# Kernel optimization log

Hardware: AMD Instinct MI355X
Metric: run time of the kernel (lower is better)

The kernel has to match this reference:

```python
import jax, jax.numpy as jnp
import numpy as np

E = 8        # num_local_experts
H = 2048     # hidden_size
I = 4096     # intermediate_size
TOP_K = 1    # num_experts_per_tok
B, S = 2, 1024


def setup_inputs() -> dict:
    key = jax.random.key(0)
    ks = jax.random.split(key, 8)
    sc = 0.02
    return {
        "hidden_states": jax.random.normal(ks[0], (B, S, H), dtype=jnp.float32),
        "router_w": jax.random.normal(ks[1], (E, H), dtype=jnp.float32) * sc,      # torch Linear weight [out,in]
        "gate_up_proj": jax.random.normal(ks[2], (E, H, 2 * I), dtype=jnp.float32) * sc,
        "down_proj": jax.random.normal(ks[3], (E, I, H), dtype=jnp.float32) * sc,
        "shared_gate": jax.random.normal(ks[4], (H, I), dtype=jnp.float32) * sc,
        "shared_up": jax.random.normal(ks[5], (H, I), dtype=jnp.float32) * sc,
        "shared_down": jax.random.normal(ks[6], (I, H), dtype=jnp.float32) * sc,
    }


def reference(hidden_states, router_w, gate_up_proj, down_proj, shared_gate, shared_up, shared_down):
    x = hidden_states.reshape(-1, H)                      # [T, H]
    T = x.shape[0]

    # Router: top-k logits kept, rest -> -inf, then sigmoid (Llama4 sigmoid routing)
    logits = jnp.einsum('th,eh->te', x, router_w)          # [T, E]
    topv, topi = jax.lax.top_k(logits, TOP_K)
    scores = jnp.full_like(logits, -jnp.inf)
    scores = scores.at[jnp.arange(T)[:, None], topi].set(topv)
    router_scores = jax.nn.sigmoid(scores.astype(jnp.float32)).astype(x.dtype).T  # [E, T]

    # Dense dispatch: every token goes to every expert, scaled by its (mostly-zero) score
    routed_in = x[None, :, :] * router_scores[:, :, None]  # [E, T, H]

    # Per-expert gated MLP as one grouped einsum
    gu = jnp.einsum('eth,ehf->etf', routed_in, gate_up_proj)   # [E, T, 2I]
    gate, up = gu[..., :I], gu[..., I:]
    routed_out = jnp.einsum('eti,eih->eth', jax.nn.silu(gate) * up, down_proj)  # [E, T, H]

    # Shared expert on raw tokens
    shared = (jax.nn.silu(x @ shared_gate) * (x @ shared_up)) @ shared_down     # [T, H]

    # scatter_add over full index range == sum over expert axis
    out = shared + routed_out.sum(axis=0)
    return out, router_scores
```

## Files before the change

### kernel.cpp

```cpp
#include <hip/hip_runtime.h>
#include <hip/hip_bf16.h>

#define NE 8
#define TT 2048
#define HD 2048
#define ID 4096

typedef __attribute__((ext_vector_type(8))) short bf16x8;
typedef __attribute__((ext_vector_type(4))) float f32x4;
typedef __attribute__((ext_vector_type(4))) unsigned int u32x4;
typedef __attribute__((ext_vector_type(2))) unsigned int u32x2;
typedef __attribute__((ext_vector_type(4))) unsigned short u16x4;

__device__ __forceinline__ unsigned short f2bf(float f) {
  unsigned int u = __builtin_bit_cast(unsigned int, f);
  u += 0x7FFFu + ((u >> 16) & 1u);
  return (unsigned short)(u >> 16);
}

__global__ void init_kernel(int* counts) {
  if (threadIdx.x < NE) counts[threadIdx.x] = 0;
}

__global__ __launch_bounds__(256) void router_kernel(
    const float* __restrict__ x, const float* __restrict__ rw,
    float* __restrict__ rs_out, unsigned short* __restrict__ xb,
    unsigned short* __restrict__ xsb, int* __restrict__ counts,
    int* __restrict__ tlist) {
  const int t = blockIdx.x;
  const int tid = threadIdx.x;
  const float* xr = x + (size_t)t * HD;
  float acc[NE];
#pragma unroll
  for (int e = 0; e < NE; ++e) acc[e] = 0.f;
  for (int h = tid; h < HD; h += 256) {
    float xv = xr[h];
#pragma unroll
    for (int e = 0; e < NE; ++e) acc[e] += xv * rw[e * HD + h];
  }
#pragma unroll
  for (int e = 0; e < NE; ++e) {
#pragma unroll
    for (int off = 32; off > 0; off >>= 1) acc[e] += __shfl_down(acc[e], off);
  }
  __shared__ float part[4][NE];
  __shared__ int sE;
  __shared__ float sS;
  const int wave = tid >> 6, lane = tid & 63;
  if (lane == 0) {
#pragma unroll
    for (int e = 0; e < NE; ++e) part[wave][e] = acc[e];
  }
  __syncthreads();
  if (tid == 0) {
    float best = -3.4e38f;
    int be = 0;
#pragma unroll
    for (int e = 0; e < NE; ++e) {
      float v = part[0][e] + part[1][e] + part[2][e] + part[3][e];
      if (v > best) { best = v; be = e; }
    }
    float s = 1.f / (1.f + expf(-best));
    sE = be;
    sS = s;
    int pos = atomicAdd(&counts[be], 1);
    tlist[be * TT + pos] = t;
  }
  __syncthreads();
  if (tid < NE) rs_out[tid * TT + t] = (tid == sE) ? sS : 0.f;
  const float s = sS;
  for (int h = tid; h < HD; h += 256) {
    float f = xr[h];
    xb[(size_t)t * HD + h] = f2bf(f);
    xsb[(size_t)t * HD + h] = f2bf(f * s);
  }
}

__global__ __launch_bounds__(256) void gateup_kernel(
    const unsigned short* __restrict__ xb, const unsigned short* __restrict__ xsb,
    const float* __restrict__ gup, const float* __restrict__ shg,
    const float* __restrict__ shu, const int* __restrict__ counts,
    const int* __restrict__ tlist, unsigned short* __restrict__ hsh,
    unsigned short* __restrict__ hrt) {
  const int bz = blockIdx.z;
  const bool sh = (bz == NE);
  const int cnt = sh ? TT : counts[bz];
  const int row0 = blockIdx.y * 128;
  if (row0 >= cnt) return;
  const int n0 = blockIdx.x * 64;
  const unsigned short* Aptr = sh ? xb : xsb;
  const float* B1;
  const float* B2;
  size_t ldb;
  if (sh) {
    B1 = shg + n0; B2 = shu + n0; ldb = ID;
  } else {
    const float* base = gup + (size_t)bz * HD * 2 * ID;
    B1 = base + n0; B2 = base + ID + n0; ldb = 2 * ID;
  }
  unsigned short* hout = sh ? hsh : hrt;

  __shared__ int toks[128];
  __shared__ __align__(16) unsigned short As[128][40];
  __shared__ __align__(16) unsigned short Bg[64][36];
  __shared__ __align__(16) unsigned short Bu[64][36];

  const int tid = threadIdx.x;
  if (tid < 128) {
    int r = row0 + tid;
    toks[tid] = (r < cnt) ? (sh ? r : tlist[bz * TT + r]) : -1;
  }
  __syncthreads();

  const int lane = tid & 63;
  const int wave = tid >> 6;
  const int wm = (wave >> 1) * 64, wn = (wave & 1) * 32;
  const int rA0 = tid >> 2, cA = (tid & 3) * 8, rA1 = rA0 + 64;
  const int tok0 = toks[rA0], tok1 = toks[rA1];
  const int nB = tid & 63;
  const int fm = lane & 15, q = lane >> 4;

  const f32x4 zf = {0.f, 0.f, 0.f, 0.f};
  f32x4 accg[4][2], accu[4][2];
#pragma unroll
  for (int a = 0; a < 4; ++a)
#pragma unroll
    for (int b = 0; b < 2; ++b) { accg[a][b] = zf; accu[a][b] = zf; }

  for (int k0 = 0; k0 < HD; k0 += 32) {
    u32x4 v0 = {0, 0, 0, 0}, v1 = {0, 0, 0, 0};
    if (tok0 >= 0) v0 = *(const u32x4*)(const void*)(Aptr + (size_t)tok0 * HD + k0 + cA);
    if (tok1 >= 0) v1 = *(const u32x4*)(const void*)(Aptr + (size_t)tok1 * HD + k0 + cA);
    *(u32x4*)(void*)&As[rA0][cA] = v0;
    *(u32x4*)(void*)&As[rA1][cA] = v1;
#pragma unroll
    for (int i = 0; i < 2; ++i) {
      const int kq = (tid >> 6) + 4 * i;
      const float* p1 = B1 + (size_t)(k0 + kq * 4) * ldb + nB;
      u16x4 w1;
      w1[0] = f2bf(p1[0]); w1[1] = f2bf(p1[ldb]);
      w1[2] = f2bf(p1[2 * ldb]); w1[3] = f2bf(p1[3 * ldb]);
      *(u16x4*)(void*)&Bg[nB][kq * 4] = w1;
      const float* p2 = B2 + (size_t)(k0 + kq * 4) * ldb + nB;
      u16x4 w2;
      w2[0] = f2bf(p2[0]); w2[1] = f2bf(p2[ldb]);
      w2[2] = f2bf(p2[2 * ldb]); w2[3] = f2bf(p2[3 * ldb]);
      *(u16x4*)(void*)&Bu[nB][kq * 4] = w2;
    }
    __syncthreads();
    bf16x8 af[4];
#pragma unroll
    for (int mt = 0; mt < 4; ++mt)
      af[mt] = __builtin_bit_cast(bf16x8,
               *(const u32x4*)(const void*)&As[wm + mt * 16 + fm][q * 8]);
    bf16x8 bgf[2], buf2[2];
#pragma unroll
    for (int nt = 0; nt < 2; ++nt) {
      const unsigned short* bp = &Bg[wn + nt * 16 + fm][q * 8];
      u32x2 lo = *(const u32x2*)(const void*)bp;
      u32x2 hi = *(const u32x2*)(const void*)(bp + 4);
      u32x4 v; v[0] = lo[0]; v[1] = lo[1]; v[2] = hi[0]; v[3] = hi[1];
      bgf[nt] = __builtin_bit_cast(bf16x8, v);
      const unsigned short* bp2 = &Bu[wn + nt * 16 + fm][q * 8];
      lo = *(const u32x2*)(const void*)bp2;
      hi = *(const u32x2*)(const void*)(bp2 + 4);
      v[0] = lo[0]; v[1] = lo[1]; v[2] = hi[0]; v[3] = hi[1];
      buf2[nt] = __builtin_bit_cast(bf16x8, v);
    }
#pragma unroll
    for (int mt = 0; mt < 4; ++mt)
#pragma unroll
      for (int nt = 0; nt < 2; ++nt) {
        accg[mt][nt] = __builtin_amdgcn_mfma_f32_16x16x32_bf16(af[mt], bgf[nt], accg[mt][nt], 0, 0, 0);
        accu[mt][nt] = __builtin_amdgcn_mfma_f32_16x16x32_bf16(af[mt], buf2[nt], accu[mt][nt], 0, 0, 0);
      }
    __syncthreads();
  }
#pragma unroll
  for (int mt = 0; mt < 4; ++mt)
#pragma unroll
    for (int nt = 0; nt < 2; ++nt)
#pragma unroll
      for (int r = 0; r < 4; ++r) {
        int ml = wm + mt * 16 + q * 4 + r;
        if (row0 + ml < cnt) {
          int tok = toks[ml];
          int n = n0 + wn + nt * 16 + fm;
          float g = accg[mt][nt][r], u = accu[mt][nt][r];
          float hv = g / (1.f + __expf(-g)) * u;
          hout[(size_t)tok * ID + n] = f2bf(hv);
        }
      }
}

__global__ __launch_bounds__(256) void down_kernel(
    const unsigned short* __restrict__ Ah, const float* __restrict__ Bbase,
    const int* __restrict__ counts, const int* __restrict__ tlist,
    float* __restrict__ out, const int routed) {
  const int e = blockIdx.z;
  const int cnt = routed ? counts[e] : TT;
  const int row0 = blockIdx.y * 128;
  if (row0 >= cnt) return;
  const int n0 = blockIdx.x * 64;
  const float* B = routed ? (Bbase + (size_t)e * ID * HD + n0) : (Bbase + n0);

  __shared__ int toks[128];
  __shared__ __align__(16) unsigned short As[128][40];
  __shared__ __align__(16) unsigned short Bs[64][36];

  const int tid = threadIdx.x;
  if (tid < 128) {
    int r = row0 + tid;
    toks[tid] = (r < cnt) ? (routed ? tlist[e * TT + r] : r) : -1;
  }
  __syncthreads();

  const int lane = tid & 63, wave = tid >> 6;
  const int wm = (wave >> 1) * 64, wn = (wave & 1) * 32;
  const int rA0 = tid >> 2, cA = (tid & 3) * 8, rA1 = rA0 + 64;
  const int tok0 = toks[rA0], tok1 = toks[rA1];
  const int nB = tid & 63;
  const int fm = lane & 15, q = lane >> 4;

  const f32x4 zf = {0.f, 0.f, 0.f, 0.f};
  f32x4 acc[4][2];
#pragma unroll
  for (int a = 0; a < 4; ++a)
#pragma unroll
    for (int b = 0; b < 2; ++b) acc[a][b] = zf;

  for (int k0 = 0; k0 < ID; k0 += 32) {
    u32x4 v0 = {0, 0, 0, 0}, v1 = {0, 0, 0, 0};
    if (tok0 >= 0) v0 = *(const u32x4*)(const void*)(Ah + (size_t)tok0 * ID + k0 + cA);
    if (tok1 >= 0) v1 = *(const u32x4*)(const void*)(Ah + (size_t)tok1 * ID + k0 + cA);
    *(u32x4*)(void*)&As[rA0][cA] = v0;
    *(u32x4*)(void*)&As[rA1][cA] = v1;
#pragma unroll
    for (int i = 0; i < 2; ++i) {
      const int kq = (tid >> 6) + 4 * i;
      const float* p = B + (size_t)(k0 + kq * 4) * HD + nB;
      u16x4 w;
      w[0] = f2bf(p[0]); w[1] = f2bf(p[HD]);
      w[2] = f2bf(p[2 * HD]); w[3] = f2bf(p[3 * HD]);
      *(u16x4*)(void*)&Bs[nB][kq * 4] = w;
    }
    __syncthreads();
    bf16x8 af[4];
#pragma unroll
    for (int mt = 0; mt < 4; ++mt)
      af[mt] = __builtin_bit_cast(bf16x8,
               *(const u32x4*)(const void*)&As[wm + mt * 16 + fm][q * 8]);
    bf16x8 bfr[2];
#pragma unroll
    for (int nt = 0; nt < 2; ++nt) {
      const unsigned short* bp = &Bs[wn + nt * 16 + fm][q * 8];
      u32x2 lo = *(const u32x2*)(const void*)bp;
      u32x2 hi = *(const u32x2*)(const void*)(bp + 4);
      u32x4 v; v[0] = lo[0]; v[1] = lo[1]; v[2] = hi[0]; v[3] = hi[1];
      bfr[nt] = __builtin_bit_cast(bf16x8, v);
    }
#pragma unroll
    for (int mt = 0; mt < 4; ++mt)
#pragma unroll
      for (int nt = 0; nt < 2; ++nt)
        acc[mt][nt] = __builtin_amdgcn_mfma_f32_16x16x32_bf16(af[mt], bfr[nt], acc[mt][nt], 0, 0, 0);
    __syncthreads();
  }
#pragma unroll
  for (int mt = 0; mt < 4; ++mt)
#pragma unroll
    for (int nt = 0; nt < 2; ++nt)
#pragma unroll
      for (int r = 0; r < 4; ++r) {
        int ml = wm + mt * 16 + q * 4 + r;
        if (row0 + ml < cnt) {
          int tok = toks[ml];
          int n = n0 + wn + nt * 16 + fm;
          float v = acc[mt][nt][r];
          float* o = out + (size_t)tok * HD + n;
          if (routed) *o += v; else *o = v;
        }
      }
}

extern "C" void kernel_launch(void* const* d_in, const int* in_sizes, int n_in,
                              void* d_out, int out_size, void* d_ws, size_t ws_size,
                              hipStream_t stream) {
  const float* x   = (const float*)d_in[0];
  const float* rw  = (const float*)d_in[1];
  const float* gup = (const float*)d_in[2];
  const float* dwn = (const float*)d_in[3];
  const float* shg = (const float*)d_in[4];
  const float* shu = (const float*)d_in[5];
  const float* shd = (const float*)d_in[6];
  float* out = (float*)d_out;

  char* ws = (char*)d_ws;
  int* counts = (int*)ws;
  int* tlist = (int*)(ws + 1024);
  unsigned short* xb  = (unsigned short*)(ws + (1 << 17));
  unsigned short* xsb = (unsigned short*)(ws + (1 << 17) + 8388608);
  unsigned short* hsh = (unsigned short*)(ws + (1 << 17) + 16777216);
  unsigned short* hrt = (unsigned short*)(ws + (1 << 17) + 33554432);

  hipLaunchKernelGGL(init_kernel, dim3(1), dim3(64), 0, stream, counts);
  hipLaunchKernelGGL(router_kernel, dim3(TT), dim3(256), 0, stream,
                     x, rw, out + (size_t)TT * HD, xb, xsb, counts, tlist);
  hipLaunchKernelGGL(gateup_kernel, dim3(ID / 64, TT / 128, NE + 1), dim3(256), 0, stream,
                     xb, xsb, gup, shg, shu, counts, tlist, hsh, hrt);
  hipLaunchKernelGGL(down_kernel, dim3(HD / 64, TT / 128, 1), dim3(256), 0, stream,
                     hsh, shd, counts, tlist, out, 0);
  hipLaunchKernelGGL(down_kernel, dim3(HD / 64, TT / 128, NE), dim3(256), 0, stream,
                     hrt, dwn, counts, tlist, out, 1);
}
```

Baseline: 1.447 ms.

## Double-buffer GEMM LDS tiles and pre-convert shared-expert weights to transposed bf16

Both GEMM kernels now keep two LDS buffers and prefetch global data two K-steps ahead into registers, so each K-step needs one barrier instead of two, and wave priority is raised around the MFMA block. A new conversion kernel transposes the shared-expert weights into bf16 once per call. The shared-expert B tiles are then read with 16-byte loads instead of strided fp32 loads converted in-loop. LDS row padding changes so B fragments can be read with a single 16-byte load. This costs an extra conversion pass over the three shared weight matrices and more workspace, and it is only enabled when the workspace is large enough.

After: 1.351 ms. 1.07x faster.

```diff
diff --git a/kernel.cpp b/kernel.cpp
--- a/kernel.cpp
+++ b/kernel.cpp
@@ -9,8 +9,8 @@
 typedef __attribute__((ext_vector_type(8))) short bf16x8;
 typedef __attribute__((ext_vector_type(4))) float f32x4;
 typedef __attribute__((ext_vector_type(4))) unsigned int u32x4;
-typedef __attribute__((ext_vector_type(2))) unsigned int u32x2;
 typedef __attribute__((ext_vector_type(4))) unsigned short u16x4;
+typedef __attribute__((ext_vector_type(8))) unsigned short u16x8;
 
 __device__ __forceinline__ unsigned short f2bf(float f) {
   unsigned int u = __builtin_bit_cast(unsigned int, f);
@@ -76,12 +76,49 @@
   }
 }
 
+__global__ __launch_bounds__(256) void tconv_kernel(
+    const float* __restrict__ shg, const float* __restrict__ shu,
+    const float* __restrict__ shd, unsigned short* __restrict__ shgT,
+    unsigned short* __restrict__ shuT, unsigned short* __restrict__ shdT) {
+  const int z = blockIdx.z;
+  const float* src;
+  unsigned short* dst;
+  int K, N;
+  if (z == 0)      { src = shg; dst = shgT; K = HD; N = ID; }
+  else if (z == 1) { src = shu; dst = shuT; K = HD; N = ID; }
+  else             { src = shd; dst = shdT; K = ID; N = HD; }
+  const int kb = blockIdx.y * 64, nb = blockIdx.x * 64;
+  if (kb >= K || nb >= N) return;
+  __shared__ unsigned short tile[64][68];
+  const int tid = threadIdx.x;
+  const int rr = tid >> 4, cc = (tid & 15) * 4;
+#pragma unroll
+  for (int it = 0; it < 4; ++it) {
+    int r = rr + it * 16;
+    f32x4 v = *(const f32x4*)(const void*)(src + (size_t)(kb + r) * N + nb + cc);
+    tile[r][cc + 0] = f2bf(v[0]);
+    tile[r][cc + 1] = f2bf(v[1]);
+    tile[r][cc + 2] = f2bf(v[2]);
+    tile[r][cc + 3] = f2bf(v[3]);
+  }
+  __syncthreads();
+  const int nr = tid >> 2, kc = (tid & 3) * 16;
+#pragma unroll
+  for (int h = 0; h < 2; ++h) {
+    u16x8 w;
+#pragma unroll
+    for (int j = 0; j < 8; ++j) w[j] = tile[kc + h * 8 + j][nr];
+    *(u16x8*)(void*)(dst + (size_t)(nb + nr) * K + kb + kc + h * 8) = w;
+  }
+}
+
 __global__ __launch_bounds__(256) void gateup_kernel(
     const unsigned short* __restrict__ xb, const unsigned short* __restrict__ xsb,
     const float* __restrict__ gup, const float* __restrict__ shg,
-    const float* __restrict__ shu, const int* __restrict__ counts,
+    const float* __restrict__ shu, const unsigned short* __restrict__ shgT,
+    const unsigned short* __restrict__ shuT, const int* __restrict__ counts,
     const int* __restrict__ tlist, unsigned short* __restrict__ hsh,
-    unsigned short* __restrict__ hrt) {
+    unsigned short* __restrict__ hrt, const int shbf) {
   const int bz = blockIdx.z;
   const bool sh = (bz == NE);
   const int cnt = sh ? TT : counts[bz];
@@ -89,11 +126,13 @@
   if (row0 >= cnt) return;
   const int n0 = blockIdx.x * 64;
   const unsigned short* Aptr = sh ? xb : xsb;
-  const float* B1;
-  const float* B2;
+  const bool bfb = sh && (shbf != 0);
+  const float *B1, *B2;
   size_t ldb;
+  const unsigned short *T1 = nullptr, *T2 = nullptr;
   if (sh) {
     B1 = shg + n0; B2 = shu + n0; ldb = ID;
+    T1 = shgT + (size_t)n0 * HD; T2 = shuT + (size_t)n0 * HD;
   } else {
     const float* base = gup + (size_t)bz * HD * 2 * ID;
     B1 = base + n0; B2 = base + ID + n0; ldb = 2 * ID;
@@ -101,9 +140,9 @@
   unsigned short* hout = sh ? hsh : hrt;
 
   __shared__ int toks[128];
-  __shared__ __align__(16) unsigned short As[128][40];
-  __shared__ __align__(16) unsigned short Bg[64][36];
-  __shared__ __align__(16) unsigned short Bu[64][36];
+  __shared__ __align__(16) unsigned short As[2][128][40];
+  __shared__ __align__(16) unsigned short Bg[2][64][40];
+  __shared__ __align__(16) unsigned short Bu[2][64][40];
 
   const int tid = threadIdx.x;
   if (tid < 128) {
@@ -112,61 +151,91 @@
   }
   __syncthreads();
 
-  const int lane = tid & 63;
-  const int wave = tid >> 6;
+  const int lane = tid & 63, wave = tid >> 6;
   const int wm = (wave >> 1) * 64, wn = (wave & 1) * 32;
   const int rA0 = tid >> 2, cA = (tid & 3) * 8, rA1 = rA0 + 64;
   const int tok0 = toks[rA0], tok1 = toks[rA1];
+  const unsigned short* ap0 = Aptr + ((tok0 >= 0) ? (size_t)tok0 * HD : 0) + cA;
+  const unsigned short* ap1 = Aptr + ((tok1 >= 0) ? (size_t)tok1 * HD : 0) + cA;
   const int nB = tid & 63;
+  const int kq0 = tid >> 6;
   const int fm = lane & 15, q = lane >> 4;
+  const int nrT = tid >> 2, kcT = (tid & 3) * 8;
 
   const f32x4 zf = {0.f, 0.f, 0.f, 0.f};
+  const u32x4 z4 = {0u, 0u, 0u, 0u};
   f32x4 accg[4][2], accu[4][2];
 #pragma unroll
   for (int a = 0; a < 4; ++a)
 #pragma unroll
     for (int b = 0; b < 2; ++b) { accg[a][b] = zf; accu[a][b] = zf; }
 
-  for (int k0 = 0; k0 < HD; k0 += 32) {
-    u32x4 v0 = {0, 0, 0, 0}, v1 = {0, 0, 0, 0};
-    if (tok0 >= 0) v0 = *(const u32x4*)(const void*)(Aptr + (size_t)tok0 * HD + k0 + cA);
-    if (tok1 >= 0) v1 = *(const u32x4*)(const void*)(Aptr + (size_t)tok1 * HD + k0 + cA);
-    *(u32x4*)(void*)&As[rA0][cA] = v0;
-    *(u32x4*)(void*)&As[rA1][cA] = v1;
-#pragma unroll
-    for (int i = 0; i < 2; ++i) {
-      const int kq = (tid >> 6) + 4 * i;
-      const float* p1 = B1 + (size_t)(k0 + kq * 4) * ldb + nB;
-      u16x4 w1;
-      w1[0] = f2bf(p1[0]); w1[1] = f2bf(p1[ldb]);
-      w1[2] = f2bf(p1[2 * ldb]); w1[3] = f2bf(p1[3 * ldb]);
-      *(u16x4*)(void*)&Bg[nB][kq * 4] = w1;
-      const float* p2 = B2 + (size_t)(k0 + kq * 4) * ldb + nB;
-      u16x4 w2;
-      w2[0] = f2bf(p2[0]); w2[1] = f2bf(p2[ldb]);
-      w2[2] = f2bf(p2[2 * ldb]); w2[3] = f2bf(p2[3 * ldb]);
-      *(u16x4*)(void*)&Bu[nB][kq * 4] = w2;
-    }
-    __syncthreads();
-    bf16x8 af[4];
+  u32x4 ra0, ra1, tb1, tb2;
+  f32x4 rg0, rg1, ru0, ru1;
+
+#define GU_LOAD(K0)                                                            \
+  do {                                                                         \
+    ra0 = (tok0 >= 0) ? *(const u32x4*)(const void*)(ap0 + (K0)) : z4;         \
+    ra1 = (tok1 >= 0) ? *(const u32x4*)(const void*)(ap1 + (K0)) : z4;         \
+    if (bfb) {                                                                 \
+      tb1 = *(const u32x4*)(const void*)(T1 + (size_t)nrT * HD + (K0) + kcT);  \
+      tb2 = *(const u32x4*)(const void*)(T2 + (size_t)nrT * HD + (K0) + kcT);  \
+    } else {                                                                   \
+      const float* p1 = B1 + (size_t)((K0) + kq0 * 4) * ldb + nB;              \
+      const float* p1b = p1 + 16 * ldb;                                        \
+      rg0[0] = p1[0]; rg0[1] = p1[ldb]; rg0[2] = p1[2 * ldb]; rg0[3] = p1[3 * ldb]; \
+      rg1[0] = p1b[0]; rg1[1] = p1b[ldb]; rg1[2] = p1b[2 * ldb]; rg1[3] = p1b[3 * ldb]; \
+      const float* p2 = B2 + (size_t)((K0) + kq0 * 4) * ldb + nB;              \
+      const float* p2b = p2 + 16 * ldb;                                        \
+      ru0[0] = p2[0]; ru0[1] = p2[ldb]; ru0[2] = p2[2 * ldb]; ru0[3] = p2[3 * ldb]; \
+      ru1[0] = p2b[0]; ru1[1] = p2b[ldb]; ru1[2] = p2b[2 * ldb]; ru1[3] = p2b[3 * ldb]; \
+    }                                                                          \
+  } while (0)
+
+#define GU_WRITE(BUF)                                                          \
+  do {                                                                         \
+    *(u32x4*)(void*)&As[BUF][rA0][cA] = ra0;                                   \
+    *(u32x4*)(void*)&As[BUF][rA1][cA] = ra1;                                   \
+    if (bfb) {                                                                 \
+      *(u32x4*)(void*)&Bg[BUF][nrT][kcT] = tb1;                                \
+      *(u32x4*)(void*)&Bu[BUF][nrT][kcT] = tb2;                                \
+    } else {                                                                   \
+      u16x4 w;                                                                 \
+      w[0] = f2bf(rg0[0]); w[1] = f2bf(rg0[1]); w[2] = f2bf(rg0[2]); w[3] = f2bf(rg0[3]); \
+      *(u16x4*)(void*)&Bg[BUF][nB][kq0 * 4] = w;                               \
+      w[0] = f2bf(rg1[0]); w[1] = f2bf(rg1[1]); w[2] = f2bf(rg1[2]); w[3] = f2bf(rg1[3]); \
+      *(u16x4*)(void*)&Bg[BUF][nB][kq0 * 4 + 16] = w;                          \
+      w[0] = f2bf(ru0[0]); w[1] = f2bf(ru0[1]); w[2] = f2bf(ru0[2]); w[3] = f2bf(ru0[3]); \
+      *(u16x4*)(void*)&Bu[BUF][nB][kq0 * 4] = w;                               \
+      w[0] = f2bf(ru1[0]); w[1] = f2bf(ru1[1]); w[2] = f2bf(ru1[2]); w[3] = f2bf(ru1[3]); \
+      *(u16x4*)(void*)&Bu[BUF][nB][kq0 * 4 + 16] = w;                          \
+    }                                                                          \
+  } while (0)
+
+  GU_LOAD(0);
+  GU_WRITE(0);
+  GU_LOAD(32);
+  asm volatile("s_waitcnt lgkmcnt(0)" ::: "memory");
+  __builtin_amdgcn_sched_barrier(0);
+  __builtin_amdgcn_s_barrier();
+
+  for (int t = 0; t < HD / 32; ++t) {
+    const int cur = t & 1;
+    bf16x8 af[4], bgf[2], buf2[2];
 #pragma unroll
     for (int mt = 0; mt < 4; ++mt)
       af[mt] = __builtin_bit_cast(bf16x8,
-               *(const u32x4*)(const void*)&As[wm + mt * 16 + fm][q * 8]);
-    bf16x8 bgf[2], buf2[2];
+               *(const u32x4*)(const void*)&As[cur][wm + mt * 16 + fm][q * 8]);
 #pragma unroll
     for (int nt = 0; nt < 2; ++nt) {
-      const unsigned short* bp = &Bg[wn + nt * 16 + fm][q * 8];
-      u32x2 lo = *(const u32x2*)(const void*)bp;
-      u32x2 hi = *(const u32x2*)(const void*)(bp + 4);
-      u32x4 v; v[0] = lo[0]; v[1] = lo[1]; v[2] = hi[0]; v[3] = hi[1];
-      bgf[nt] = __builtin_bit_cast(bf16x8, v);
-      const unsigned short* bp2 = &Bu[wn + nt * 16 + fm][q * 8];
-      lo = *(const u32x2*)(const void*)bp2;
-      hi = *(const u32x2*)(const void*)(bp2 + 4);
-      v[0] = lo[0]; v[1] = lo[1]; v[2] = hi[0]; v[3] = hi[1];
-      buf2[nt] = __builtin_bit_cast(bf16x8, v);
+      bgf[nt] = __builtin_bit_cast(bf16x8,
+                *(const u32x4*)(const void*)&Bg[cur][wn + nt * 16 + fm][q * 8]);
+      buf2[nt] = __builtin_bit_cast(bf16x8,
+                 *(const u32x4*)(const void*)&Bu[cur][wn + nt * 16 + fm][q * 8]);
     }
+    if (t + 1 < HD / 32) GU_WRITE(cur ^ 1);
+    if (t + 2 < HD / 32) GU_LOAD((t + 2) * 32);
+    __builtin_amdgcn_s_setprio(1);
 #pragma unroll
     for (int mt = 0; mt < 4; ++mt)
 #pragma unroll
@@ -174,8 +243,14 @@
         accg[mt][nt] = __builtin_amdgcn_mfma_f32_16x16x32_bf16(af[mt], bgf[nt], accg[mt][nt], 0, 0, 0);
         accu[mt][nt] = __builtin_amdgcn_mfma_f32_16x16x32_bf16(af[mt], buf2[nt], accu[mt][nt], 0, 0, 0);
       }
-    __syncthreads();
-  }
+    __builtin_amdgcn_s_setprio(0);
+    asm volatile("s_waitcnt lgkmcnt(0)" ::: "memory");
+    __builtin_amdgcn_sched_barrier(0);
+    __builtin_amdgcn_s_barrier();
+  }
+#undef GU_LOAD
+#undef GU_WRITE
+
 #pragma unroll
   for (int mt = 0; mt < 4; ++mt)
 #pragma unroll
@@ -195,18 +270,21 @@
 
 __global__ __launch_bounds__(256) void down_kernel(
     const unsigned short* __restrict__ Ah, const float* __restrict__ Bbase,
-    const int* __restrict__ counts, const int* __restrict__ tlist,
-    float* __restrict__ out, const int routed) {
+    const unsigned short* __restrict__ BT, const int* __restrict__ counts,
+    const int* __restrict__ tlist, float* __restrict__ out,
+    const int routed, const int shbf) {
   const int e = blockIdx.z;
   const int cnt = routed ? counts[e] : TT;
   const int row0 = blockIdx.y * 128;
   if (row0 >= cnt) return;
   const int n0 = blockIdx.x * 64;
+  const bool bfb = (!routed) && (shbf != 0);
   const float* B = routed ? (Bbase + (size_t)e * ID * HD + n0) : (Bbase + n0);
+  const unsigned short* T = BT + (size_t)n0 * ID;
 
   __shared__ int toks[128];
-  __shared__ __align__(16) unsigned short As[128][40];
-  __shared__ __align__(16) unsigned short Bs[64][36];
+  __shared__ __align__(16) unsigned short As[2][128][40];
+  __shared__ __align__(16) unsigned short Bs[2][64][40];
 
   const int tid = threadIdx.x;
   if (tid < 128) {
@@ -219,53 +297,87 @@
   const int wm = (wave >> 1) * 64, wn = (wave & 1) * 32;
   const int rA0 = tid >> 2, cA = (tid & 3) * 8, rA1 = rA0 + 64;
   const int tok0 = toks[rA0], tok1 = toks[rA1];
+  const unsigned short* ap0 = Ah + ((tok0 >= 0) ? (size_t)tok0 * ID : 0) + cA;
+  const unsigned short* ap1 = Ah + ((tok1 >= 0) ? (size_t)tok1 * ID : 0) + cA;
   const int nB = tid & 63;
+  const int kq0 = tid >> 6;
   const int fm = lane & 15, q = lane >> 4;
+  const int nrT = tid >> 2, kcT = (tid & 3) * 8;
 
   const f32x4 zf = {0.f, 0.f, 0.f, 0.f};
+  const u32x4 z4 = {0u, 0u, 0u, 0u};
   f32x4 acc[4][2];
 #pragma unroll
   for (int a = 0; a < 4; ++a)
 #pragma unroll
     for (int b = 0; b < 2; ++b) acc[a][b] = zf;
 
-  for (int k0 = 0; k0 < ID; k0 += 32) {
-    u32x4 v0 = {0, 0, 0, 0}, v1 = {0, 0, 0, 0};
-    if (tok0 >= 0) v0 = *(const u32x4*)(const void*)(Ah + (size_t)tok0 * ID + k0 + cA);
-    if (tok1 >= 0) v1 = *(const u32x4*)(const void*)(Ah + (size_t)tok1 * ID + k0 + cA);
-    *(u32x4*)(void*)&As[rA0][cA] = v0;
-    *(u32x4*)(void*)&As[rA1][cA] = v1;
-#pragma unroll
-    for (int i = 0; i < 2; ++i) {
-      const int kq = (tid >> 6) + 4 * i;
-      const float* p = B + (size_t)(k0 + kq * 4) * HD + nB;
-      u16x4 w;
-      w[0] = f2bf(p[0]); w[1] = f2bf(p[HD]);
-      w[2] = f2bf(p[2 * HD]); w[3] = f2bf(p[3 * HD]);
-      *(u16x4*)(void*)&Bs[nB][kq * 4] = w;
-    }
-    __syncthreads();
-    bf16x8 af[4];
+  u32x4 ra0, ra1, tb;
+  f32x4 rb0, rb1;
+
+#define DN_LOAD(K0)                                                            \
+  do {                                                                         \
+    ra0 = (tok0 >= 0) ? *(const u32x4*)(const void*)(ap0 + (K0)) : z4;         \
+    ra1 = (tok1 >= 0) ? *(const u32x4*)(const void*)(ap1 + (K0)) : z4;         \
+    if (bfb) {                                                                 \
+      tb = *(const u32x4*)(const void*)(T + (size_t)nrT * ID + (K0) + kcT);    \
+    } else {                                                                   \
+      const float* p = B + (size_t)((K0) + kq0 * 4) * HD + nB;                 \
+      const float* pb = p + 16 * HD;                                           \
+      rb0[0] = p[0]; rb0[1] = p[HD]; rb0[2] = p[2 * HD]; rb0[3] = p[3 * HD];   \
+      rb1[0] = pb[0]; rb1[1] = pb[HD]; rb1[2] = pb[2 * HD]; rb1[3] = pb[3 * HD]; \
+    }                                                                          \
+  } while (0)
+
+#define DN_WRITE(BUF)                                                          \
+  do {                                                                         \
+    *(u32x4*)(void*)&As[BUF][rA0][cA] = ra0;                                   \
+    *(u32x4*)(void*)&As[BUF][rA1][cA] = ra1;                                   \
+    if (bfb) {                                                                 \
+      *(u32x4*)(void*)&Bs[BUF][nrT][kcT] = tb;                                 \
+    } else {                                                                   \
+      u16x4 w;                                                                 \
+      w[0] = f2bf(rb0[0]); w[1] = f2bf(rb0[1]); w[2] = f2bf(rb0[2]); w[3] = f2bf(rb0[3]); \
+      *(u16x4*)(void*)&Bs[BUF][nB][kq0 * 4] = w;                               \
+      w[0] = f2bf(rb1[0]); w[1] = f2bf(rb1[1]); w[2] = f2bf(rb1[2]); w[3] = f2bf(rb1[3]); \
+      *(u16x4*)(void*)&Bs[BUF][nB][kq0 * 4 + 16] = w;                          \
+    }                                                                          \
+  } while (0)
+
+  DN_LOAD(0);
+  DN_WRITE(0);
+  DN_LOAD(32);
+  asm volatile("s_waitcnt lgkmcnt(0)" ::: "memory");
+  __builtin_amdgcn_sched_barrier(0);
+  __builtin_amdgcn_s_barrier();
+
+  for (int t = 0; t < ID / 32; ++t) {
+    const int cur = t & 1;
+    bf16x8 af[4], bfr[2];
 #pragma unroll
     for (int mt = 0; mt < 4; ++mt)
       af[mt] = __builtin_bit_cast(bf16x8,
-               *(const u32x4*)(const void*)&As[wm + mt * 16 + fm][q * 8]);
-    bf16x8 bfr[2];
-#pragma unroll
-    for (int nt = 0; nt < 2; ++nt) {
-      const unsigned short* bp = &Bs[wn + nt * 16 + fm][q * 8];
-      u32x2 lo = *(const u32x2*)(const void*)bp;
-      u32x2 hi = *(const u32x2*)(const void*)(bp + 4);
-      u32x4 v; v[0] = lo[0]; v[1] = lo[1]; v[2] = hi[0]; v[3] = hi[1];
-      bfr[nt] = __builtin_bit_cast(bf16x8, v);
-    }
+               *(const u32x4*)(const void*)&As[cur][wm + mt * 16 + fm][q * 8]);
+#pragma unroll
+    for (int nt = 0; nt < 2; ++nt)
+      bfr[nt] = __builtin_bit_cast(bf16x8,
+                *(const u32x4*)(const void*)&Bs[cur][wn + nt * 16 + fm][q * 8]);
+    if (t + 1 < ID / 32) DN_WRITE(cur ^ 1);
+    if (t + 2 < ID / 32) DN_LOAD((t + 2) * 32);
+    __builtin_amdgcn_s_setprio(1);
 #pragma unroll
     for (int mt = 0; mt < 4; ++mt)
 #pragma unroll
       for (int nt = 0; nt < 2; ++nt)
         acc[mt][nt] = __builtin_amdgcn_mfma_f32_16x16x32_bf16(af[mt], bfr[nt], acc[mt][nt], 0, 0, 0);
-    __syncthreads();
-  }
+    __builtin_amdgcn_s_setprio(0);
+    asm volatile("s_waitcnt lgkmcnt(0)" ::: "memory");
+    __builtin_amdgcn_sched_barrier(0);
+    __builtin_amdgcn_s_barrier();
+  }
+#undef DN_LOAD
+#undef DN_WRITE
+
 #pragma unroll
   for (int mt = 0; mt < 4; ++mt)
 #pragma unroll
@@ -302,14 +414,23 @@
   unsigned short* xsb = (unsigned short*)(ws + (1 << 17) + 8388608);
   unsigned short* hsh = (unsigned short*)(ws + (1 << 17) + 16777216);
   unsigned short* hrt = (unsigned short*)(ws + (1 << 17) + 33554432);
+  const size_t WB = (size_t)(1 << 17) + 50331648;
+  unsigned short* shgT = (unsigned short*)(ws + WB);
+  unsigned short* shuT = (unsigned short*)(ws + WB + 16777216);
+  unsigned short* shdT = (unsigned short*)(ws + WB + 33554432);
+  const size_t need = WB + 3ull * 16777216ull;
+  const int shbf = (ws_size >= need) ? 1 : 0;
 
   hipLaunchKernelGGL(init_kernel, dim3(1), dim3(64), 0, stream, counts);
   hipLaunchKernelGGL(router_kernel, dim3(TT), dim3(256), 0, stream,
                      x, rw, out + (size_t)TT * HD, xb, xsb, counts, tlist);
+  if (shbf)
+    hipLaunchKernelGGL(tconv_kernel, dim3(64, 64, 3), dim3(256), 0, stream,
+                       shg, shu, shd, shgT, shuT, shdT);
   hipLaunchKernelGGL(gateup_kernel, dim3(ID / 64, TT / 128, NE + 1), dim3(256), 0, stream,
-                     xb, xsb, gup, shg, shu, counts, tlist, hsh, hrt);
+                     xb, xsb, gup, shg, shu, shgT, shuT, counts, tlist, hsh, hrt, shbf);
   hipLaunchKernelGGL(down_kernel, dim3(HD / 64, TT / 128, 1), dim3(256), 0, stream,
-                     hsh, shd, counts, tlist, out, 0);
+                     hsh, shd, shdT, counts, tlist, out, 0, shbf);
   hipLaunchKernelGGL(down_kernel, dim3(HD / 64, TT / 128, NE), dim3(256), 0, stream,
-                     hrt, dwn, counts, tlist, out, 1);
-}
+                     hrt, dwn, shdT, counts, tlist, out, 1, shbf);
+}
```
